# Kernel optimization log

Measured on AMD Instinct MI355X. Metric: run time of the kernel, lower is better.

The kernel has to match this reference:

```python
import jax, jax.numpy as jnp
import numpy as np

B, M, D = 4, 2048, 1024
N, P = 64, 32  # num_experts, slots_per_expert


def setup_inputs() -> dict:
    key = jax.random.key(0)
    k1, k2, k3, k4 = jax.random.split(key, 4)
    x = jax.random.normal(k1, (B, M, D), dtype=jnp.float32)
    phi = jax.random.normal(k2, (D, N, P), dtype=jnp.float32) * (1.0 / np.sqrt(D))
    W = jax.random.normal(k3, (N, D, D), dtype=jnp.float32) * (1.0 / np.sqrt(D))
    b = jax.random.normal(k4, (N, D), dtype=jnp.float32) * 0.01
    return {"x": x, "phi": phi, "W": W, "b": b}


def reference(x, phi, W, b):
    # logits: (b, m, n, p)
    logits = jnp.einsum('bmd,dnp->bmnp', x, phi)
    # dispatch: softmax over dim=0 (batch), faithful to the given source
    dispatch = jax.nn.softmax(logits, axis=0)
    # combine: softmax over flattened (n*p) slot axis
    bsz, m, n, p = logits.shape
    combine = jax.nn.softmax(logits.reshape(bsz, m, n * p), axis=-1).reshape(bsz, m, n, p)
    # slot inputs: (b, n, p, d)
    slots = jnp.einsum('bmd,bmnp->bnpd', x, dispatch)
    # per-expert GEMM + bias
    y = jnp.einsum('bnpd,nde->bnpe', slots, W) + b[None, :, None, :]
    # combine back to tokens: (b, m, d)
    out = jnp.einsum('bnpd,bmnp->bmd', y, combine)
    return out
```

## Files before the change

### kernel.cpp

```cpp
#include <hip/hip_runtime.h>
#include <hip/hip_bf16.h>
#include <cstddef>

#define Bb 4
#define Mm 2048
#define Dd 1024
#define Nn 64
#define Pp 32
#define NP 2048
#define BM 8192

typedef __attribute__((ext_vector_type(4))) float v4f;
typedef __attribute__((ext_vector_type(8))) short v8s;

__device__ inline unsigned short f2b(float f) {
  union { float f; unsigned u; } v; v.f = f;
  unsigned r = v.u + 0x7fff + ((v.u >> 16) & 1);
  return (unsigned short)(r >> 16);
}

__device__ inline void gld16(const void* g, void* l) {
  __builtin_amdgcn_global_load_lds(
      (const __attribute__((address_space(1))) unsigned*)g,
      (__attribute__((address_space(3))) unsigned*)l, 16, 0, 0);
}

__global__ __launch_bounds__(256) void k_xprep(const float* __restrict__ x,
                                               unsigned short* __restrict__ xb,
                                               unsigned short* __restrict__ xT) {
  __shared__ unsigned short t[32][33];
  const int b = blockIdx.z;
  const int r0 = blockIdx.y * 32;
  const int c0 = blockIdx.x * 32;
  const float* ib = x + (size_t)b * Mm * Dd;
  const int tr = threadIdx.x >> 3;
  const int tc = (threadIdx.x & 7) * 4;
  float4 v = *(const float4*)&ib[(size_t)(r0 + tr) * Dd + c0 + tc];
  ushort4 s;
  s.x = f2b(v.x); s.y = f2b(v.y); s.z = f2b(v.z); s.w = f2b(v.w);
  *(ushort4*)&xb[(size_t)b * Mm * Dd + (size_t)(r0 + tr) * Dd + c0 + tc] = s;
  t[tr][tc + 0] = s.x; t[tr][tc + 1] = s.y;
  t[tr][tc + 2] = s.z; t[tr][tc + 3] = s.w;
  __syncthreads();
  ushort4 o;
  o.x = t[tc + 0][tr]; o.y = t[tc + 1][tr];
  o.z = t[tc + 2][tr]; o.w = t[tc + 3][tr];
  *(ushort4*)&xT[(size_t)b * Dd * Mm + (size_t)(c0 + tr) * Mm + r0 + tc] = o;
}

__global__ __launch_bounds__(256) void k_tr_f2b(const float* __restrict__ in,
                                                unsigned short* __restrict__ out,
                                                int R, int C) {
  __shared__ unsigned short t[32][33];
  const int r0 = blockIdx.y * 32, c0 = blockIdx.x * 32;
  const int tr = threadIdx.x >> 3;
  const int tc = (threadIdx.x & 7) * 4;
  float4 v = *(const float4*)&in[(size_t)(r0 + tr) * C + c0 + tc];
  t[tr][tc + 0] = f2b(v.x); t[tr][tc + 1] = f2b(v.y);
  t[tr][tc + 2] = f2b(v.z); t[tr][tc + 3] = f2b(v.w);
  __syncthreads();
  ushort4 o;
  o.x = t[tc + 0][tr]; o.y = t[tc + 1][tr];
  o.z = t[tc + 2][tr]; o.w = t[tc + 3][tr];
  *(ushort4*)&out[(size_t)(c0 + tr) * R + r0 + tc] = o;
}

__global__ __launch_bounds__(256) void k_tr_b2b(const unsigned short* __restrict__ in, size_t sin_,
                                                unsigned short* __restrict__ out, size_t sout,
                                                int R, int C) {
  __shared__ unsigned short t[32][33];
  const int r0 = blockIdx.y * 32, c0 = blockIdx.x * 32;
  const unsigned short* ib = in + (size_t)blockIdx.z * sin_;
  unsigned short* ob = out + (size_t)blockIdx.z * sout;
  const int tr = threadIdx.x >> 3;
  const int tc = (threadIdx.x & 7) * 4;
  ushort4 v = *(const ushort4*)&ib[(size_t)(r0 + tr) * C + c0 + tc];
  t[tr][tc + 0] = v.x; t[tr][tc + 1] = v.y;
  t[tr][tc + 2] = v.z; t[tr][tc + 3] = v.w;
  __syncthreads();
  ushort4 o;
  o.x = t[tc + 0][tr]; o.y = t[tc + 1][tr];
  o.z = t[tc + 2][tr]; o.w = t[tc + 3][tr];
  *(ushort4*)&ob[(size_t)(c0 + tr) * R + r0 + tc] = o;
}

template <int OUT_BF16>
__global__ __launch_bounds__(512, 2) void k_gemm8(const unsigned short* __restrict__ A, size_t sA,
                                                  const unsigned short* __restrict__ B, size_t sB,
                                                  void* __restrict__ C, size_t sC,
                                                  int M, int N, int K, int nbx) {
  __shared__ unsigned short As[4][256][32];
  __shared__ unsigned short Bs[4][256][32];
  const int nwg = (int)gridDim.x;
  const int bid = (int)blockIdx.x;
  const int swz = (bid & 7) * (nwg >> 3) + (bid >> 3);
  const int bx = swz % nbx, by = swz / nbx;
  const int tid = threadIdx.x;
  const int wv = tid >> 6, ln = tid & 63;
  const int wm = wv >> 2, wn = wv & 3;
  const int row0 = by * 256, col0 = bx * 256;
  const unsigned short* Ab = A + (size_t)blockIdx.z * sA + (size_t)row0 * K;
  const unsigned short* Bbp = B + (size_t)blockIdx.z * sB + (size_t)col0 * K;
  const int srow = wv * 32 + (ln >> 2);
  const int ssc = (ln & 3) * 8;
  const int fr = ln & 15, fc = (ln >> 4) * 8;
  const int nt = K >> 5;
  v4f acc[8][4];
#pragma unroll
  for (int i = 0; i < 8; ++i)
#pragma unroll
    for (int j = 0; j < 4; ++j) { v4f z = {0.f, 0.f, 0.f, 0.f}; acc[i][j] = z; }

#define STAGE8(t, buf) do {                                        \
    size_t ga1 = (size_t)srow * K + (size_t)(t) * 32 + ssc;        \
    size_t ga2 = ga1 + (size_t)16 * K;                             \
    gld16(Ab + ga1,  &As[buf][wv * 32][0]);                        \
    gld16(Ab + ga2,  &As[buf][wv * 32 + 16][0]);                   \
    gld16(Bbp + ga1, &Bs[buf][wv * 32][0]);                        \
    gld16(Bbp + ga2, &Bs[buf][wv * 32 + 16][0]);                   \
  } while (0)

#define COMP8(buf) do {                                            \
    v8s a[8], b[4];                                                \
    _Pragma("unroll")                                              \
    for (int i = 0; i < 8; ++i)                                    \
      a[i] = *(const v8s*)&As[buf][wm * 128 + 16 * i + fr][fc];    \
    _Pragma("unroll")                                              \
    for (int j = 0; j < 4; ++j)                                    \
      b[j] = *(const v8s*)&Bs[buf][wn * 64 + 16 * j + fr][fc];     \
    __builtin_amdgcn_s_setprio(1);                                 \
    _Pragma("unroll")                                              \
    for (int i = 0; i < 8; ++i)                                    \
      _Pragma("unroll")                                            \
      for (int j = 0; j < 4; ++j)                                  \
        acc[i][j] = __builtin_amdgcn_mfma_f32_16x16x32_bf16(a[i], b[j], acc[i][j], 0, 0, 0); \
    __builtin_amdgcn_s_setprio(0);                                 \
  } while (0)

  STAGE8(0, 0);
  STAGE8(1, 1);
  STAGE8(2, 2);
  asm volatile("s_waitcnt vmcnt(8)" ::: "memory");
  __builtin_amdgcn_s_barrier();
  __builtin_amdgcn_sched_barrier(0);

  for (int t = 0; t < nt - 3; ++t) {
    STAGE8(t + 3, (t + 3) & 3);
    COMP8(t & 3);
    asm volatile("s_waitcnt vmcnt(8)" ::: "memory");
    __builtin_amdgcn_s_barrier();
    __builtin_amdgcn_sched_barrier(0);
  }
  COMP8((nt - 3) & 3);
  asm volatile("s_waitcnt vmcnt(4)" ::: "memory");
  __builtin_amdgcn_s_barrier();
  __builtin_amdgcn_sched_barrier(0);
  COMP8((nt - 2) & 3);
  asm volatile("s_waitcnt vmcnt(0)" ::: "memory");
  __builtin_amdgcn_s_barrier();
  __builtin_amdgcn_sched_barrier(0);
  COMP8((nt - 1) & 3);
#undef STAGE8
#undef COMP8

  const int er = (ln >> 4) * 4, ec = ln & 15;
#pragma unroll
  for (int i = 0; i < 8; ++i)
#pragma unroll
    for (int j = 0; j < 4; ++j) {
      int r = row0 + wm * 128 + 16 * i + er;
      int c = col0 + wn * 64 + 16 * j + ec;
      if (OUT_BF16) {
        unsigned short* Cp = (unsigned short*)C + (size_t)blockIdx.z * sC + (size_t)r * N + c;
#pragma unroll
        for (int q = 0; q < 4; ++q) Cp[(size_t)q * N] = f2b(acc[i][j][q]);
      } else {
        float* Cp = (float*)C + (size_t)blockIdx.z * sC + (size_t)r * N + c;
#pragma unroll
        for (int q = 0; q < 4; ++q) Cp[(size_t)q * N] = acc[i][j][q];
      }
    }
}

__global__ __launch_bounds__(256) void k_softmax(const float* __restrict__ logits,
                                                 unsigned short* __restrict__ dispatch,
                                                 unsigned short* __restrict__ combine) {
  __shared__ float sh[Bb][NP];
  __shared__ float redm[Bb][4];
  __shared__ float reds[Bb][4];
  const int m = blockIdx.x;
  const int tid = threadIdx.x;
  const int wv = tid >> 6, ln = tid & 63;
#pragma unroll
  for (int b = 0; b < Bb; ++b) {
    const float4* src = (const float4*)(logits + ((size_t)b * Mm + m) * NP);
#pragma unroll
    for (int it = 0; it < 2; ++it) ((float4*)sh[b])[tid + it * 256] = src[tid + it * 256];
  }
  __syncthreads();
#pragma unroll
  for (int it = 0; it < 8; ++it) {
    int np = tid + it * 256;
    float v0 = sh[0][np], v1 = sh[1][np], v2 = sh[2][np], v3 = sh[3][np];
    float mx = fmaxf(fmaxf(v0, v1), fmaxf(v2, v3));
    float e0 = __expf(v0 - mx), e1 = __expf(v1 - mx);
    float e2 = __expf(v2 - mx), e3 = __expf(v3 - mx);
    float inv = 1.0f / (e0 + e1 + e2 + e3);
    dispatch[((size_t)0 * Mm + m) * NP + np] = f2b(e0 * inv);
    dispatch[((size_t)1 * Mm + m) * NP + np] = f2b(e1 * inv);
    dispatch[((size_t)2 * Mm + m) * NP + np] = f2b(e2 * inv);
    dispatch[((size_t)3 * Mm + m) * NP + np] = f2b(e3 * inv);
  }
#pragma unroll
  for (int b = 0; b < Bb; ++b) {
    float lmax = -3.0e38f;
#pragma unroll
    for (int it = 0; it < 8; ++it) lmax = fmaxf(lmax, sh[b][tid + it * 256]);
#pragma unroll
    for (int o = 32; o > 0; o >>= 1) lmax = fmaxf(lmax, __shfl_xor(lmax, o, 64));
    if (ln == 0) redm[b][wv] = lmax;
    __syncthreads();
    float mx = fmaxf(fmaxf(redm[b][0], redm[b][1]), fmaxf(redm[b][2], redm[b][3]));
    float lsum = 0.0f;
#pragma unroll
    for (int it = 0; it < 8; ++it) {
      int np = tid + it * 256;
      float e = __expf(sh[b][np] - mx);
      sh[b][np] = e;
      lsum += e;
    }
#pragma unroll
    for (int o = 32; o > 0; o >>= 1) lsum += __shfl_xor(lsum, o, 64);
    if (ln == 0) reds[b][wv] = lsum;
    __syncthreads();
    float inv = 1.0f / (reds[b][0] + reds[b][1] + reds[b][2] + reds[b][3]);
#pragma unroll
    for (int it = 0; it < 8; ++it) {
      int np = tid + it * 256;
      combine[((size_t)b * Mm + m) * NP + np] = f2b(sh[b][np] * inv);
    }
  }
}

__global__ __launch_bounds__(256) void k_y_mfma(const unsigned short* __restrict__ slots,
                                                const float* __restrict__ W,
                                                const float* __restrict__ bias,
                                                unsigned short* __restrict__ y) {
  __shared__ unsigned short As[2][128][32];
  __shared__ unsigned short Bs[2][128][40];
  const int n = blockIdx.z;
  const int col0 = blockIdx.x * 128;
  const int tid = threadIdx.x;
  const int wv = tid >> 6, ln = tid & 63;
  const int wm = wv & 1, wn = wv >> 1;
  const int sr = ln >> 2, sc = (ln & 3) * 8;
  const int fr = ln & 15, fc = (ln >> 4) * 8;
  const float* Wn = W + (size_t)n * Dd * Dd;
  v4f acc[4][4];
#pragma unroll
  for (int i = 0; i < 4; ++i)
#pragma unroll
    for (int j = 0; j < 4; ++j) { v4f z = {0.f, 0.f, 0.f, 0.f}; acc[i][j] = z; }

  for (int kt = 0; kt < Dd; kt += 64) {
    __syncthreads();
    {
      int r1 = 32 * wv + sr;
      int r2 = r1 + 16;
      size_t g1 = ((size_t)(r1 >> 5) * NP + n * Pp + (r1 & 31)) * Dd + kt + sc;
      size_t g2 = ((size_t)(r2 >> 5) * NP + n * Pp + (r2 & 31)) * Dd + kt + sc;
      gld16(slots + g1,      &As[0][32 * wv][0]);
      gld16(slots + g2,      &As[0][32 * wv + 16][0]);
      gld16(slots + g1 + 32, &As[1][32 * wv][0]);
      gld16(slots + g2 + 32, &As[1][32 * wv + 16][0]);
    }
#pragma unroll
    for (int buf = 0; buf < 2; ++buf) {
#pragma unroll
      for (int it = 0; it < 2; ++it) {
        int idx = tid + it * 256;
        int k = ((idx >> 2) & 15) * 2;
        int eseg = ((idx & 3) + ((idx >> 6) << 2)) * 4;
        const float* wp = &Wn[(size_t)(kt + buf * 32 + k) * Dd + col0 + eseg];
        float4 r0 = *(const float4*)wp;
        float4 r1 = *(const float4*)(wp + Dd);
        *(__hip_bfloat162*)&Bs[buf][eseg + 0][k] = __float22bfloat162_rn(float2{r0.x, r1.x});
        *(__hip_bfloat162*)&Bs[buf][eseg + 1][k] = __float22bfloat162_rn(float2{r0.y, r1.y});
        *(__hip_bfloat162*)&Bs[buf][eseg + 2][k] = __float22bfloat162_rn(float2{r0.z, r1.z});
        *(__hip_bfloat162*)&Bs[buf][eseg + 3][k] = __float22bfloat162_rn(float2{r0.w, r1.w});
      }
    }
    __syncthreads();
#pragma unroll
    for (int ks = 0; ks < 2; ++ks) {
      v8s a[4], b[4];
#pragma unroll
      for (int i = 0; i < 4; ++i) a[i] = *(const v8s*)&As[ks][64 * wm + 16 * i + fr][fc];
#pragma unroll
      for (int j = 0; j < 4; ++j) b[j] = *(const v8s*)&Bs[ks][64 * wn + 16 * j + fr][fc];
#pragma unroll
      for (int i = 0; i < 4; ++i)
#pragma unroll
        for (int j = 0; j < 4; ++j)
          acc[i][j] = __builtin_amdgcn_mfma_f32_16x16x32_bf16(a[i], b[j], acc[i][j], 0, 0, 0);
    }
  }
  const int er = (ln >> 4) * 4, ec = ln & 15;
  float bv[4];
#pragma unroll
  for (int j = 0; j < 4; ++j) bv[j] = bias[(size_t)n * Dd + col0 + 64 * wn + 16 * j + ec];
#pragma unroll
  for (int i = 0; i < 4; ++i)
#pragma unroll
    for (int j = 0; j < 4; ++j) {
      int c = col0 + 64 * wn + 16 * j + ec;
#pragma unroll
      for (int q = 0; q < 4; ++q) {
        int r = 64 * wm + 16 * i + er + q;
        size_t row = (size_t)(r >> 5) * NP + n * Pp + (r & 31);
        y[row * Dd + c] = f2b(acc[i][j][q] + bv[j]);
      }
    }
}

extern "C" void kernel_launch(void* const* d_in, const int* in_sizes, int n_in,
                              void* d_out, int out_size, void* d_ws, size_t ws_size,
                              hipStream_t stream) {
  const float* x    = (const float*)d_in[0];
  const float* phi  = (const float*)d_in[1];
  const float* W    = (const float*)d_in[2];
  const float* bias = (const float*)d_in[3];
  float* out = (float*)d_out;
  char* ws = (char*)d_ws;

  float*          logits = (float*)(ws);
  unsigned short* disp_b = (unsigned short*)(ws + 67108864);
  unsigned short* comb_b = (unsigned short*)(ws + 100663296);
  unsigned short* dispT  = (unsigned short*)(ws + 134217728);
  unsigned short* xb     = (unsigned short*)(ws + 167772160);
  unsigned short* xT     = (unsigned short*)(ws + 184549376);
  unsigned short* phiT   = (unsigned short*)(ws + 201326592);
  unsigned short* slots  = (unsigned short*)(ws + 209715200);
  unsigned short* y_b    = (unsigned short*)(ws + 226492416);
  unsigned short* yT     = (unsigned short*)(ws + 243269632);

  k_xprep<<<dim3(32, 64, Bb), 256, 0, stream>>>(x, xb, xT);
  k_tr_f2b<<<dim3(64, 32, 1), 256, 0, stream>>>(phi, phiT, Dd, NP);
  k_gemm8<0><<<dim3(256, 1, 1), 512, 0, stream>>>(xb, 0, phiT, 0, logits, 0, BM, NP, Dd, 8);
  k_softmax<<<Mm, 256, 0, stream>>>(logits, disp_b, comb_b);
  k_tr_b2b<<<dim3(64, 64, Bb), 256, 0, stream>>>(disp_b, (size_t)Mm * NP, dispT, (size_t)NP * Mm, Mm, NP);
  k_gemm8<1><<<dim3(32, 1, Bb), 512, 0, stream>>>(dispT, (size_t)NP * Mm, xT, (size_t)Dd * Mm,
                                                  slots, (size_t)NP * Dd, NP, Dd, Mm, 4);
  k_y_mfma<<<dim3(8, 1, Nn), 256, 0, stream>>>(slots, W, bias, y_b);
  k_tr_b2b<<<dim3(32, 64, Bb), 256, 0, stream>>>(y_b, (size_t)NP * Dd, yT, (size_t)Dd * NP, NP, Dd);
  k_gemm8<0><<<dim3(32, 1, Bb), 512, 0, stream>>>(comb_b, (size_t)Mm * NP, yT, (size_t)Dd * NP,
                                                  out, (size_t)Mm * Dd, Mm, Dd, NP, 4);
}
```

Before: 681.2 us.

## Restructure bf16 GEMM with triple-buffered swizzled LDS and split-phase MMA pipeline

Replaces the 4-stage GEMM with a templated kernel that uses 3 LDS buffers and XOR-swizzled LDS columns to avoid bank conflicts. Each K step is split into two halves that interleave the global-to-LDS loads with fragment reads and MFMAs. The two batched GEMMs (slots and output) now use 128-row tiles with twice as many workgroups to improve occupancy and CU coverage. The cost is more barriers per iteration and a smaller prefetch depth.

```diff
diff --git a/kernel.cpp b/kernel.cpp
--- a/kernel.cpp
+++ b/kernel.cpp
@@ -84,91 +84,122 @@
   *(ushort4*)&ob[(size_t)(c0 + tr) * R + r0 + tc] = o;
 }
 
-template <int OUT_BF16>
-__global__ __launch_bounds__(512, 2) void k_gemm8(const unsigned short* __restrict__ A, size_t sA,
-                                                  const unsigned short* __restrict__ B, size_t sB,
-                                                  void* __restrict__ C, size_t sC,
-                                                  int M, int N, int K, int nbx) {
-  __shared__ unsigned short As[4][256][32];
-  __shared__ unsigned short Bs[4][256][32];
+template <int MF, int OUT_BF16>
+__global__ __launch_bounds__(512) void k_g8(const unsigned short* __restrict__ A, size_t sA,
+                                            const unsigned short* __restrict__ B, size_t sB,
+                                            void* __restrict__ C, size_t sC,
+                                            int M, int N, int K, int nbx) {
+  constexpr int BMt = MF * 32;
+  constexpr int LA  = MF / 4;
+  constexpr int LPT = LA + 2;
+  __shared__ unsigned short As[3][BMt][32];
+  __shared__ unsigned short Bs[3][256][32];
   const int nwg = (int)gridDim.x;
   const int bid = (int)blockIdx.x;
   const int swz = (bid & 7) * (nwg >> 3) + (bid >> 3);
   const int bx = swz % nbx, by = swz / nbx;
-  const int tid = threadIdx.x;
+  const int tid = (int)threadIdx.x;
   const int wv = tid >> 6, ln = tid & 63;
   const int wm = wv >> 2, wn = wv & 3;
-  const int row0 = by * 256, col0 = bx * 256;
+  const int row0 = by * BMt, col0 = bx * 256;
   const unsigned short* Ab = A + (size_t)blockIdx.z * sA + (size_t)row0 * K;
   const unsigned short* Bbp = B + (size_t)blockIdx.z * sB + (size_t)col0 * K;
-  const int srow = wv * 32 + (ln >> 2);
-  const int ssc = (ln & 3) * 8;
-  const int fr = ln & 15, fc = (ln >> 4) * 8;
+  const int rowg0 = 16 * wv + (ln >> 2);
+  const int csrc = (((ln & 3) ^ ((ln & 32) ? 2 : 0)) << 3);
+  const int fr = ln & 15;
+  const int fce = (((ln >> 4) << 3) ^ ((fr & 8) ? 16 : 0));
   const int nt = K >> 5;
-  v4f acc[8][4];
-#pragma unroll
-  for (int i = 0; i < 8; ++i)
+  v4f acc[MF][4];
+#pragma unroll
+  for (int i = 0; i < MF; ++i)
 #pragma unroll
     for (int j = 0; j < 4; ++j) { v4f z = {0.f, 0.f, 0.f, 0.f}; acc[i][j] = z; }
 
-#define STAGE8(t, buf) do {                                        \
-    size_t ga1 = (size_t)srow * K + (size_t)(t) * 32 + ssc;        \
-    size_t ga2 = ga1 + (size_t)16 * K;                             \
-    gld16(Ab + ga1,  &As[buf][wv * 32][0]);                        \
-    gld16(Ab + ga2,  &As[buf][wv * 32 + 16][0]);                   \
-    gld16(Bbp + ga1, &Bs[buf][wv * 32][0]);                        \
-    gld16(Bbp + ga2, &Bs[buf][wv * 32 + 16][0]);                   \
-  } while (0)
-
-#define COMP8(buf) do {                                            \
-    v8s a[8], b[4];                                                \
-    _Pragma("unroll")                                              \
-    for (int i = 0; i < 8; ++i)                                    \
-      a[i] = *(const v8s*)&As[buf][wm * 128 + 16 * i + fr][fc];    \
-    _Pragma("unroll")                                              \
-    for (int j = 0; j < 4; ++j)                                    \
-      b[j] = *(const v8s*)&Bs[buf][wn * 64 + 16 * j + fr][fc];     \
-    __builtin_amdgcn_s_setprio(1);                                 \
-    _Pragma("unroll")                                              \
-    for (int i = 0; i < 8; ++i)                                    \
-      _Pragma("unroll")                                            \
-      for (int j = 0; j < 4; ++j)                                  \
-        acc[i][j] = __builtin_amdgcn_mfma_f32_16x16x32_bf16(a[i], b[j], acc[i][j], 0, 0, 0); \
-    __builtin_amdgcn_s_setprio(0);                                 \
-  } while (0)
-
-  STAGE8(0, 0);
-  STAGE8(1, 1);
-  STAGE8(2, 2);
-  asm volatile("s_waitcnt vmcnt(8)" ::: "memory");
-  __builtin_amdgcn_s_barrier();
+#define STG_A(t_, r_) do {                                                  \
+    size_t g0 = (size_t)rowg0 * K + (size_t)(t_) * 32 + csrc;               \
+    gld16(Ab + g0, &As[r_][16 * wv][0]);                                    \
+    if (LA == 2) gld16(Ab + g0 + (size_t)128 * K, &As[r_][16 * wv + 128][0]); \
+  } while (0)
+#define STG_B(t_, r_) do {                                                  \
+    size_t g0 = (size_t)rowg0 * K + (size_t)(t_) * 32 + csrc;               \
+    gld16(Bbp + g0, &Bs[r_][16 * wv][0]);                                   \
+    gld16(Bbp + g0 + (size_t)128 * K, &Bs[r_][16 * wv + 128][0]);           \
+  } while (0)
+#define RD_B(r_) do {                                                       \
+    _Pragma("unroll")                                                       \
+    for (int j = 0; j < 4; ++j)                                             \
+      bfr[j] = *(const v8s*)&Bs[r_][wn * 64 + 16 * j + fr][fce];            \
+  } while (0)
+#define RD_A(r_, half_) do {                                                \
+    _Pragma("unroll")                                                       \
+    for (int i = 0; i < MF / 2; ++i)                                        \
+      afr[i] = *(const v8s*)&As[r_][wm * (MF * 16) + 16 * ((half_) * (MF / 2) + i) + fr][fce]; \
+  } while (0)
+#define MMA(half_) do {                                                     \
+    __builtin_amdgcn_s_setprio(1);                                          \
+    _Pragma("unroll")                                                       \
+    for (int i = 0; i < MF / 2; ++i)                                        \
+      _Pragma("unroll")                                                     \
+      for (int j = 0; j < 4; ++j)                                           \
+        acc[(half_) * (MF / 2) + i][j] =                                    \
+            __builtin_amdgcn_mfma_f32_16x16x32_bf16(afr[i], bfr[j],         \
+                acc[(half_) * (MF / 2) + i][j], 0, 0, 0);                   \
+    __builtin_amdgcn_s_setprio(0);                                          \
+  } while (0)
+#define IRON(n_) asm volatile("s_waitcnt vmcnt(" #n_ ")\n\ts_barrier" ::: "memory")
+
+  STG_A(0, 0); STG_B(0, 0);
+  STG_A(1, 1); STG_B(1, 1);
+  if constexpr (LPT == 4) IRON(4); else IRON(3);
   __builtin_amdgcn_sched_barrier(0);
 
-  for (int t = 0; t < nt - 3; ++t) {
-    STAGE8(t + 3, (t + 3) & 3);
-    COMP8(t & 3);
-    asm volatile("s_waitcnt vmcnt(8)" ::: "memory");
+  int rc = 0;
+  for (int t = 0; t < nt - 2; ++t) {
+    int rn = rc + 2; if (rn >= 3) rn -= 3;
+    v8s bfr[4], afr[MF / 2];
+    STG_A(t + 2, rn);
+    RD_B(rc);
+    RD_A(rc, 0);
     __builtin_amdgcn_s_barrier();
     __builtin_amdgcn_sched_barrier(0);
-  }
-  COMP8((nt - 3) & 3);
-  asm volatile("s_waitcnt vmcnt(4)" ::: "memory");
-  __builtin_amdgcn_s_barrier();
-  __builtin_amdgcn_sched_barrier(0);
-  COMP8((nt - 2) & 3);
-  asm volatile("s_waitcnt vmcnt(0)" ::: "memory");
-  __builtin_amdgcn_s_barrier();
-  __builtin_amdgcn_sched_barrier(0);
-  COMP8((nt - 1) & 3);
-#undef STAGE8
-#undef COMP8
+    MMA(0);
+    __builtin_amdgcn_sched_barrier(0);
+    __builtin_amdgcn_s_barrier();
+    STG_B(t + 2, rn);
+    RD_A(rc, 1);
+    if constexpr (LPT == 4) IRON(4); else IRON(3);
+    __builtin_amdgcn_sched_barrier(0);
+    MMA(1);
+    __builtin_amdgcn_sched_barrier(0);
+    __builtin_amdgcn_s_barrier();
+    rc = rc + 1; if (rc >= 3) rc -= 3;
+  }
+  {
+    v8s bfr[4], afr[MF / 2];
+    RD_B(rc); RD_A(rc, 0); MMA(0);
+    RD_A(rc, 1); MMA(1);
+    IRON(0);
+    __builtin_amdgcn_sched_barrier(0);
+    rc = rc + 1; if (rc >= 3) rc -= 3;
+  }
+  {
+    v8s bfr[4], afr[MF / 2];
+    RD_B(rc); RD_A(rc, 0); MMA(0);
+    RD_A(rc, 1); MMA(1);
+  }
+#undef STG_A
+#undef STG_B
+#undef RD_B
+#undef RD_A
+#undef MMA
+#undef IRON
 
   const int er = (ln >> 4) * 4, ec = ln & 15;
 #pragma unroll
-  for (int i = 0; i < 8; ++i)
+  for (int i = 0; i < MF; ++i)
 #pragma unroll
     for (int j = 0; j < 4; ++j) {
-      int r = row0 + wm * 128 + 16 * i + er;
+      int r = row0 + wm * (MF * 16) + 16 * i + er;
       int c = col0 + wn * 64 + 16 * j + ec;
       if (OUT_BF16) {
         unsigned short* Cp = (unsigned short*)C + (size_t)blockIdx.z * sC + (size_t)r * N + c;
@@ -346,13 +377,13 @@
 
   k_xprep<<<dim3(32, 64, Bb), 256, 0, stream>>>(x, xb, xT);
   k_tr_f2b<<<dim3(64, 32, 1), 256, 0, stream>>>(phi, phiT, Dd, NP);
-  k_gemm8<0><<<dim3(256, 1, 1), 512, 0, stream>>>(xb, 0, phiT, 0, logits, 0, BM, NP, Dd, 8);
+  k_g8<8, 0><<<dim3(256, 1, 1), 512, 0, stream>>>(xb, 0, phiT, 0, logits, 0, BM, NP, Dd, 8);
   k_softmax<<<Mm, 256, 0, stream>>>(logits, disp_b, comb_b);
   k_tr_b2b<<<dim3(64, 64, Bb), 256, 0, stream>>>(disp_b, (size_t)Mm * NP, dispT, (size_t)NP * Mm, Mm, NP);
-  k_gemm8<1><<<dim3(32, 1, Bb), 512, 0, stream>>>(dispT, (size_t)NP * Mm, xT, (size_t)Dd * Mm,
+  k_g8<4, 1><<<dim3(64, 1, Bb), 512, 0, stream>>>(dispT, (size_t)NP * Mm, xT, (size_t)Dd * Mm,
                                                   slots, (size_t)NP * Dd, NP, Dd, Mm, 4);
   k_y_mfma<<<dim3(8, 1, Nn), 256, 0, stream>>>(slots, W, bias, y_b);
   k_tr_b2b<<<dim3(32, 64, Bb), 256, 0, stream>>>(y_b, (size_t)NP * Dd, yT, (size_t)Dd * NP, NP, Dd);
-  k_gemm8<0><<<dim3(32, 1, Bb), 512, 0, stream>>>(comb_b, (size_t)Mm * NP, yT, (size_t)Dd * NP,
+  k_g8<4, 0><<<dim3(64, 1, Bb), 512, 0, stream>>>(comb_b, (size_t)Mm * NP, yT, (size_t)Dd * NP,
                                                   out, (size_t)Mm * Dd, Mm, Dd, NP, 4);
 }
```

New measurement: 657.7 us. 3.4% less time.
